# Optimization experiments

Hardware: AMD Instinct MI355X
Metric: run time of the kernel (lower is better)

## Reference

```python
import jax, jax.numpy as jnp
import numpy as np

B = 65536

def setup_inputs() -> dict:
    key = jax.random.key(0)
    ks = jax.random.split(key, 6)
    x = jax.random.normal(ks[0], (B, 784), dtype=jnp.float32)
    w_conv = jnp.ones((3, 3), dtype=jnp.float32)  # Parameter(ones((3,3)))
    w1 = jax.random.normal(ks[1], (676, 256), dtype=jnp.float32) * 0.04
    b1 = jax.random.normal(ks[2], (256,), dtype=jnp.float32) * 0.01
    w2 = jax.random.normal(ks[3], (256, 10), dtype=jnp.float32) * 0.06
    b2 = jax.random.normal(ks[4], (10,), dtype=jnp.float32) * 0.01
    return {"x": x, "w_conv": w_conv, "w1": w1, "b1": b1, "w2": w2, "b2": b2}

def reference(x, w_conv, w1, b1, w2, b2):
    b = x.shape[0]
    img = x.reshape(b, 1, 28, 28)
    # Convolve() is cross-correlation (no kernel flip), 'VALID': 28->26
    kern = w_conv.reshape(1, 1, 3, 3)
    conv = jax.lax.conv_general_dilated(
        img, kern, window_strides=(1, 1), padding='VALID',
        dimension_numbers=('NCHW', 'OIHW', 'NCHW'))  # (B,1,26,26)
    feat = conv.reshape(b, 676)
    h = jax.nn.relu(feat @ w1 + b1)  # (B,256)
    return h @ w2 + b2               # (B,10)
```

## Files before the change

### kernel.cpp

```cpp
#include <hip/hip_runtime.h>
#include <hip/hip_bf16.h>
#include <stdint.h>

typedef __bf16 bf16;
typedef __attribute__((ext_vector_type(8))) __bf16 bf16x8;
typedef __attribute__((ext_vector_type(4))) float f32x4;

#define KREAL 784
#define NTILES 25
#define TROW   40
#define TILE_ELEMS (256 * TROW)

#define GLOBAL_AS __attribute__((address_space(1)))
#define LDS_AS    __attribute__((address_space(3)))

__global__ __launch_bounds__(256) void prep_w1tt(const float* __restrict__ w_conv,
                                                 const float* __restrict__ w1,
                                                 bf16* __restrict__ W) {
    const int tile = blockIdx.x / TROW;
    const int kk   = blockIdx.x % TROW;
    const int n    = threadIdx.x;
    const int k    = tile * 32 + kk;
    float s = 0.0f;
    if (kk < 32 && k < KREAL) {
        const int r = k / 28, c = k % 28;
        #pragma unroll
        for (int di = 0; di < 3; ++di) {
            const int i = r - di;
            if (i < 0 || i >= 26) continue;
            #pragma unroll
            for (int dj = 0; dj < 3; ++dj) {
                const int j = c - dj;
                if (j < 0 || j >= 26) continue;
                s += w_conv[di * 3 + dj] * w1[(i * 26 + j) * 256 + n];
            }
        }
    }
    W[(size_t)tile * TILE_ELEMS + n * TROW + kk] = (bf16)s;
}

template <int CTRL>
__device__ __forceinline__ float dpp_add(float s) {
    int v = __builtin_amdgcn_update_dpp(0, __float_as_int(s), CTRL, 0xf, 0xf, false);
    return s + __int_as_float(v);
}

__global__ __launch_bounds__(256, 2) void fused_mlp(
    const float* __restrict__ x,
    const bf16*  __restrict__ W,
    const float* __restrict__ b1,
    const float* __restrict__ w2,
    const float* __restrict__ b2,
    float* __restrict__ out)
{
    __shared__ bf16  Bs[2][TILE_ELEMS];
    __shared__ float w2s[256][10];
    __shared__ float b1s[256];
    __shared__ float b2s[10];

    const int t    = threadIdx.x;
    const int wave = t >> 6;
    const int lane = t & 63;
    const int c    = lane & 15;
    const int q    = lane >> 4;

    const int row0 = blockIdx.x * 128;

    for (int i = t; i < 2560; i += 256) ((float*)w2s)[i] = w2[i];
    b1s[t] = b1[t];
    if (t < 10) b2s[t] = b2[t];

    const float* arow0 = x + (size_t)(row0 + wave * 32 + c) * KREAL + q * 8;
    const float* arow1 = arow0 + (size_t)16 * KREAL;
    const bf16* bsrc = W + (size_t)(wave * 5) * 512 + lane * 8;

    f32x4 acc[2][16];
    #pragma unroll
    for (int mt = 0; mt < 2; ++mt)
        #pragma unroll
        for (int nt = 0; nt < 16; ++nt)
            acc[mt][nt] = (f32x4){0.f, 0.f, 0.f, 0.f};

    #pragma unroll
    for (int j = 0; j < 5; ++j) {
        __builtin_amdgcn_global_load_lds(
            (const GLOBAL_AS void*)(bsrc + j * 512),
            (LDS_AS void*)((char*)&Bs[0][0] + (wave * 5 + j) * 1024), 16, 0, 0);
    }
    float4 f0a = *(const float4*)arow0, f0b = *(const float4*)(arow0 + 4);
    float4 f1a = *(const float4*)arow1, f1b = *(const float4*)(arow1 + 4);
    bf16x8 a0, a1;
    a0[0] = (bf16)f0a.x; a0[1] = (bf16)f0a.y; a0[2] = (bf16)f0a.z; a0[3] = (bf16)f0a.w;
    a0[4] = (bf16)f0b.x; a0[5] = (bf16)f0b.y; a0[6] = (bf16)f0b.z; a0[7] = (bf16)f0b.w;
    a1[0] = (bf16)f1a.x; a1[1] = (bf16)f1a.y; a1[2] = (bf16)f1a.z; a1[3] = (bf16)f1a.w;
    a1[4] = (bf16)f1b.x; a1[5] = (bf16)f1b.y; a1[6] = (bf16)f1b.z; a1[7] = (bf16)f1b.w;
    __syncthreads();

    #pragma unroll 1
    for (int it = 0; it < NTILES; ++it) {
        const int cur = it & 1;
        const bool more = (it + 1) < NTILES;

        if (more) {
            const bf16* bs = bsrc + (size_t)(it + 1) * TILE_ELEMS;
            char* bd = (char*)&Bs[cur ^ 1][0] + wave * 5 * 1024;
            #pragma unroll
            for (int j = 0; j < 5; ++j) {
                __builtin_amdgcn_global_load_lds(
                    (const GLOBAL_AS void*)(bs + j * 512),
                    (LDS_AS void*)(bd + j * 1024), 16, 0, 0);
            }
            const int kn = (it + 1) * 32;
            if (kn + q * 8 < KREAL) {
                const float* p0 = arow0 + kn;
                const float* p1 = arow1 + kn;
                f0a = *(const float4*)p0; f0b = *(const float4*)(p0 + 4);
                f1a = *(const float4*)p1; f1b = *(const float4*)(p1 + 4);
            } else {
                f0a = f0b = f1a = f1b = (float4){0.f, 0.f, 0.f, 0.f};
            }
        }

        #pragma unroll
        for (int nt = 0; nt < 16; ++nt) {
            bf16x8 b = *(const bf16x8*)&Bs[cur][(nt * 16 + c) * TROW + q * 8];
            acc[0][nt] = __builtin_amdgcn_mfma_f32_16x16x32_bf16(a0, b, acc[0][nt], 0, 0, 0);
            acc[1][nt] = __builtin_amdgcn_mfma_f32_16x16x32_bf16(a1, b, acc[1][nt], 0, 0, 0);
        }

        if (more) {
            a0[0] = (bf16)f0a.x; a0[1] = (bf16)f0a.y; a0[2] = (bf16)f0a.z; a0[3] = (bf16)f0a.w;
            a0[4] = (bf16)f0b.x; a0[5] = (bf16)f0b.y; a0[6] = (bf16)f0b.z; a0[7] = (bf16)f0b.w;
            a1[0] = (bf16)f1a.x; a1[1] = (bf16)f1a.y; a1[2] = (bf16)f1a.z; a1[3] = (bf16)f1a.w;
            a1[4] = (bf16)f1b.x; a1[5] = (bf16)f1b.y; a1[6] = (bf16)f1b.z; a1[7] = (bf16)f1b.w;
        }

        __syncthreads();
    }

    float bl[16];
    #pragma unroll
    for (int nt = 0; nt < 16; ++nt) bl[nt] = b1s[nt * 16 + c];

    #pragma unroll
    for (int mt = 0; mt < 2; ++mt)
        #pragma unroll
        for (int nt = 0; nt < 16; ++nt)
            #pragma unroll
            for (int r = 0; r < 4; ++r) {
                float v = acc[mt][nt][r] + bl[nt];
                acc[mt][nt][r] = v > 0.f ? v : 0.f;
            }

    #pragma unroll 1
    for (int j = 0; j < 10; ++j) {
        float wj[16];
        #pragma unroll
        for (int nt = 0; nt < 16; ++nt) wj[nt] = w2s[nt * 16 + c][j];
        const float b2j = b2s[j];
        #pragma unroll
        for (int mt = 0; mt < 2; ++mt)
            #pragma unroll
            for (int r = 0; r < 4; ++r) {
                float s = 0.f;
                #pragma unroll
                for (int nt = 0; nt < 16; ++nt) s += acc[mt][nt][r] * wj[nt];
                s = dpp_add<0xB1>(s);
                s = dpp_add<0x4E>(s);
                s = dpp_add<0x124>(s);
                s = dpp_add<0x128>(s);
                if (c == j) {
                    const int row = row0 + wave * 32 + mt * 16 + q * 4 + r;
                    out[(size_t)row * 10 + j] = s + b2j;
                }
            }
    }
}

extern "C" void kernel_launch(void* const* d_in, const int* in_sizes, int n_in,
                              void* d_out, int out_size, void* d_ws, size_t ws_size,
                              hipStream_t stream) {
    const float* x  = (const float*)d_in[0];
    const float* wc = (const float*)d_in[1];
    const float* w1 = (const float*)d_in[2];
    const float* b1 = (const float*)d_in[3];
    const float* w2 = (const float*)d_in[4];
    const float* b2 = (const float*)d_in[5];
    float* out = (float*)d_out;
    bf16* W = (bf16*)d_ws;

    prep_w1tt<<<dim3(NTILES * TROW), dim3(256), 0, stream>>>(wc, w1, W);
    fused_mlp<<<dim3(65536 / 128), dim3(256), 0, stream>>>(x, W, b1, w2, b2, out);
}
```

Measured before the change: 312.5 us.

## Prefetch activation rows two K-tiles ahead with explicit waitcnt barriers

Deepens the activation prefetch from one to two tiles ahead, using ping-pong float4 register sets and a loop unrolled by two. It also replaces __syncthreads with hand-placed s_waitcnt vmcnt plus s_barrier, so the newest global loads can stay in flight across the barrier. Out-of-range K chunks are now read at offset 0 and multiplied by a zero mask instead of branching. This uses more registers and relies on exact vmcnt accounting for correctness.

```diff
diff --git a/kernel.cpp b/kernel.cpp
--- a/kernel.cpp
+++ b/kernel.cpp
@@ -81,62 +81,89 @@
         for (int nt = 0; nt < 16; ++nt)
             acc[mt][nt] = (f32x4){0.f, 0.f, 0.f, 0.f};
 
+    float4 E0, E1, E2, E3, O0, O1, O2, O3;
+    bf16x8 a0, a1;
+
     #pragma unroll
     for (int j = 0; j < 5; ++j) {
         __builtin_amdgcn_global_load_lds(
             (const GLOBAL_AS void*)(bsrc + j * 512),
             (LDS_AS void*)((char*)&Bs[0][0] + (wave * 5 + j) * 1024), 16, 0, 0);
     }
-    float4 f0a = *(const float4*)arow0, f0b = *(const float4*)(arow0 + 4);
-    float4 f1a = *(const float4*)arow1, f1b = *(const float4*)(arow1 + 4);
-    bf16x8 a0, a1;
-    a0[0] = (bf16)f0a.x; a0[1] = (bf16)f0a.y; a0[2] = (bf16)f0a.z; a0[3] = (bf16)f0a.w;
-    a0[4] = (bf16)f0b.x; a0[5] = (bf16)f0b.y; a0[6] = (bf16)f0b.z; a0[7] = (bf16)f0b.w;
-    a1[0] = (bf16)f1a.x; a1[1] = (bf16)f1a.y; a1[2] = (bf16)f1a.z; a1[3] = (bf16)f1a.w;
-    a1[4] = (bf16)f1b.x; a1[5] = (bf16)f1b.y; a1[6] = (bf16)f1b.z; a1[7] = (bf16)f1b.w;
-    __syncthreads();
+    E0 = *(const float4*)arow0;        E1 = *(const float4*)(arow0 + 4);
+    E2 = *(const float4*)arow1;        E3 = *(const float4*)(arow1 + 4);
+    O0 = *(const float4*)(arow0 + 32); O1 = *(const float4*)(arow0 + 36);
+    O2 = *(const float4*)(arow1 + 32); O3 = *(const float4*)(arow1 + 36);
+    a0[0] = (bf16)E0.x; a0[1] = (bf16)E0.y; a0[2] = (bf16)E0.z; a0[3] = (bf16)E0.w;
+    a0[4] = (bf16)E1.x; a0[5] = (bf16)E1.y; a0[6] = (bf16)E1.z; a0[7] = (bf16)E1.w;
+    a1[0] = (bf16)E2.x; a1[1] = (bf16)E2.y; a1[2] = (bf16)E2.z; a1[3] = (bf16)E2.w;
+    a1[4] = (bf16)E3.x; a1[5] = (bf16)E3.y; a1[6] = (bf16)E3.z; a1[7] = (bf16)E3.w;
+    asm volatile("s_waitcnt vmcnt(4) lgkmcnt(0)" ::: "memory");
+    __builtin_amdgcn_sched_barrier(0);
+    __builtin_amdgcn_s_barrier();
+    __builtin_amdgcn_sched_barrier(0);
+
+#define KSTEP(IT, CUR, P0, P1, P2, P3, Q0, Q1, Q2, Q3)                         \
+    do {                                                                       \
+        const int  it_    = (IT);                                              \
+        const bool more_  = (it_ + 1) < NTILES;                                \
+        const bool more2_ = (it_ + 2) < NTILES;                                \
+        if (more_) {                 \
+            const bf16* bs_ = bsrc + (size_t)(it_ + 1) * TILE_ELEMS;           \
+            char* bd_ = (char*)&Bs[(CUR) ^ 1][0] + wave * 5 * 1024;            \
+            _Pragma("unroll")                                                  \
+            for (int j = 0; j < 5; ++j) {                                      \
+                __builtin_amdgcn_global_load_lds(                              \
+                    (const GLOBAL_AS void*)(bs_ + j * 512),                    \
+                    (LDS_AS void*)(bd_ + j * 1024), 16, 0, 0);                 \
+            }                                                                  \
+        }                                                                      \
+        if (more2_) {                         \
+            const int kn_   = (it_ + 2) * 32;                                  \
+            const int koff_ = (kn_ + q * 8 < KREAL) ? kn_ : 0;                 \
+            Q0 = *(const float4*)(arow0 + koff_);                              \
+            Q1 = *(const float4*)(arow0 + koff_ + 4);                          \
+            Q2 = *(const float4*)(arow1 + koff_);                              \
+            Q3 = *(const float4*)(arow1 + koff_ + 4);                          \
+        }                                                                      \
+        {                                            \
+            const bf16* bb_ = &Bs[(CUR)][0] + c * TROW + q * 8;                \
+            _Pragma("unroll")                                                  \
+            for (int nt = 0; nt < 16; ++nt) {                                  \
+                bf16x8 b_ = *(const bf16x8*)(bb_ + nt * 16 * TROW);            \
+                acc[0][nt] = __builtin_amdgcn_mfma_f32_16x16x32_bf16(          \
+                    a0, b_, acc[0][nt], 0, 0, 0);                              \
+                acc[1][nt] = __builtin_amdgcn_mfma_f32_16x16x32_bf16(          \
+                    a1, b_, acc[1][nt], 0, 0, 0);                              \
+            }                                                                  \
+        }                                                                      \
+        if (more_) {                \
+            const float okm_ = ((it_ + 1) * 32 + q * 8 < KREAL) ? 1.f : 0.f;   \
+            a0[0] = (bf16)(P0.x * okm_); a0[1] = (bf16)(P0.y * okm_);          \
+            a0[2] = (bf16)(P0.z * okm_); a0[3] = (bf16)(P0.w * okm_);          \
+            a0[4] = (bf16)(P1.x * okm_); a0[5] = (bf16)(P1.y * okm_);          \
+            a0[6] = (bf16)(P1.z * okm_); a0[7] = (bf16)(P1.w * okm_);          \
+            a1[0] = (bf16)(P2.x * okm_); a1[1] = (bf16)(P2.y * okm_);          \
+            a1[2] = (bf16)(P2.z * okm_); a1[3] = (bf16)(P2.w * okm_);          \
+            a1[4] = (bf16)(P3.x * okm_); a1[5] = (bf16)(P3.y * okm_);          \
+            a1[6] = (bf16)(P3.z * okm_); a1[7] = (bf16)(P3.w * okm_);          \
+        }                                                                      \
+        if (more_) {                    \
+            if (more2_) asm volatile("s_waitcnt vmcnt(4)" ::: "memory");       \
+            else        asm volatile("s_waitcnt vmcnt(0)" ::: "memory");       \
+            __builtin_amdgcn_sched_barrier(0);                                 \
+            __builtin_amdgcn_s_barrier();                                      \
+            __builtin_amdgcn_sched_barrier(0);                                 \
+        }                                                                      \
+    } while (0)
 
     #pragma unroll 1
-    for (int it = 0; it < NTILES; ++it) {
-        const int cur = it & 1;
-        const bool more = (it + 1) < NTILES;
-
-        if (more) {
-            const bf16* bs = bsrc + (size_t)(it + 1) * TILE_ELEMS;
-            char* bd = (char*)&Bs[cur ^ 1][0] + wave * 5 * 1024;
-            #pragma unroll
-            for (int j = 0; j < 5; ++j) {
-                __builtin_amdgcn_global_load_lds(
-                    (const GLOBAL_AS void*)(bs + j * 512),
-                    (LDS_AS void*)(bd + j * 1024), 16, 0, 0);
-            }
-            const int kn = (it + 1) * 32;
-            if (kn + q * 8 < KREAL) {
-                const float* p0 = arow0 + kn;
-                const float* p1 = arow1 + kn;
-                f0a = *(const float4*)p0; f0b = *(const float4*)(p0 + 4);
-                f1a = *(const float4*)p1; f1b = *(const float4*)(p1 + 4);
-            } else {
-                f0a = f0b = f1a = f1b = (float4){0.f, 0.f, 0.f, 0.f};
-            }
-        }
-
-        #pragma unroll
-        for (int nt = 0; nt < 16; ++nt) {
-            bf16x8 b = *(const bf16x8*)&Bs[cur][(nt * 16 + c) * TROW + q * 8];
-            acc[0][nt] = __builtin_amdgcn_mfma_f32_16x16x32_bf16(a0, b, acc[0][nt], 0, 0, 0);
-            acc[1][nt] = __builtin_amdgcn_mfma_f32_16x16x32_bf16(a1, b, acc[1][nt], 0, 0, 0);
-        }
-
-        if (more) {
-            a0[0] = (bf16)f0a.x; a0[1] = (bf16)f0a.y; a0[2] = (bf16)f0a.z; a0[3] = (bf16)f0a.w;
-            a0[4] = (bf16)f0b.x; a0[5] = (bf16)f0b.y; a0[6] = (bf16)f0b.z; a0[7] = (bf16)f0b.w;
-            a1[0] = (bf16)f1a.x; a1[1] = (bf16)f1a.y; a1[2] = (bf16)f1a.z; a1[3] = (bf16)f1a.w;
-            a1[4] = (bf16)f1b.x; a1[5] = (bf16)f1b.y; a1[6] = (bf16)f1b.z; a1[7] = (bf16)f1b.w;
-        }
-
-        __syncthreads();
-    }
+    for (int base = 0; base < NTILES - 1; base += 2) {
+        KSTEP(base,     0, O0, O1, O2, O3, E0, E1, E2, E3);
+        KSTEP(base + 1, 1, E0, E1, E2, E3, O0, O1, O2, O3);
+    }
+    KSTEP(NTILES - 1, 0, O0, O1, O2, O3, E0, E1, E2, E3);
+#undef KSTEP
 
     float bl[16];
     #pragma unroll
```

After: 315.8 us. About the same (+1.1%).

## Split waves into 64-row pairs sharing rows, halving N per wave

Applied to the files above, without the earlier changes.

Waves are regrouped into pairs that each cover 64 rows. Within a pair, each wave computes half of the 256 hidden columns over 4 M-tiles, so a wave now does 4x8 MFMAs per tile instead of 2x16. Each B fragment read from LDS is reused across four A tiles, which halves LDS B reads per MFMA. The cost is that each wave loads four A rows instead of two, so every x row is fetched by both waves of the pair and global A traffic doubles. The second layer's partial sums are combined across the pair through LDS, which adds a barrier.

```diff
diff --git a/kernel.cpp b/kernel.cpp
--- a/kernel.cpp
+++ b/kernel.cpp
@@ -43,6 +43,13 @@
 __device__ __forceinline__ float dpp_add(float s) {
     int v = __builtin_amdgcn_update_dpp(0, __float_as_int(s), CTRL, 0xf, 0xf, false);
     return s + __int_as_float(v);
+}
+
+__device__ __forceinline__ bf16x8 cvt8(float4 lo, float4 hi) {
+    bf16x8 r;
+    r[0] = (bf16)lo.x; r[1] = (bf16)lo.y; r[2] = (bf16)lo.z; r[3] = (bf16)lo.w;
+    r[4] = (bf16)hi.x; r[5] = (bf16)hi.y; r[6] = (bf16)hi.z; r[7] = (bf16)hi.w;
+    return r;
 }
 
 __global__ __launch_bounds__(256, 2) void fused_mlp(
@@ -63,6 +70,8 @@
     const int lane = t & 63;
     const int c    = lane & 15;
     const int q    = lane >> 4;
+    const int pair = wave >> 1;
+    const int nh   = wave & 1;
 
     const int row0 = blockIdx.x * 128;
 
@@ -70,15 +79,14 @@
     b1s[t] = b1[t];
     if (t < 10) b2s[t] = b2[t];
 
-    const float* arow0 = x + (size_t)(row0 + wave * 32 + c) * KREAL + q * 8;
-    const float* arow1 = arow0 + (size_t)16 * KREAL;
+    const float* ar = x + (size_t)(row0 + pair * 64 + c) * KREAL + q * 8;
     const bf16* bsrc = W + (size_t)(wave * 5) * 512 + lane * 8;
 
-    f32x4 acc[2][16];
-    #pragma unroll
-    for (int mt = 0; mt < 2; ++mt)
-        #pragma unroll
-        for (int nt = 0; nt < 16; ++nt)
+    f32x4 acc[4][8];
+    #pragma unroll
+    for (int mt = 0; mt < 4; ++mt)
+        #pragma unroll
+        for (int nt = 0; nt < 8; ++nt)
             acc[mt][nt] = (f32x4){0.f, 0.f, 0.f, 0.f};
 
     #pragma unroll
@@ -87,13 +95,16 @@
             (const GLOBAL_AS void*)(bsrc + j * 512),
             (LDS_AS void*)((char*)&Bs[0][0] + (wave * 5 + j) * 1024), 16, 0, 0);
     }
-    float4 f0a = *(const float4*)arow0, f0b = *(const float4*)(arow0 + 4);
-    float4 f1a = *(const float4*)arow1, f1b = *(const float4*)(arow1 + 4);
-    bf16x8 a0, a1;
-    a0[0] = (bf16)f0a.x; a0[1] = (bf16)f0a.y; a0[2] = (bf16)f0a.z; a0[3] = (bf16)f0a.w;
-    a0[4] = (bf16)f0b.x; a0[5] = (bf16)f0b.y; a0[6] = (bf16)f0b.z; a0[7] = (bf16)f0b.w;
-    a1[0] = (bf16)f1a.x; a1[1] = (bf16)f1a.y; a1[2] = (bf16)f1a.z; a1[3] = (bf16)f1a.w;
-    a1[4] = (bf16)f1b.x; a1[5] = (bf16)f1b.y; a1[6] = (bf16)f1b.z; a1[7] = (bf16)f1b.w;
+    float4 fa[4], fb[4];
+    #pragma unroll
+    for (int mt = 0; mt < 4; ++mt) {
+        const float* p = ar + (size_t)(mt * 16) * KREAL;
+        fa[mt] = *(const float4*)p;
+        fb[mt] = *(const float4*)(p + 4);
+    }
+    bf16x8 a[4];
+    #pragma unroll
+    for (int mt = 0; mt < 4; ++mt) a[mt] = cvt8(fa[mt], fb[mt]);
     __syncthreads();
 
     #pragma unroll 1
@@ -112,68 +123,98 @@
             }
             const int kn = (it + 1) * 32;
             if (kn + q * 8 < KREAL) {
-                const float* p0 = arow0 + kn;
-                const float* p1 = arow1 + kn;
-                f0a = *(const float4*)p0; f0b = *(const float4*)(p0 + 4);
-                f1a = *(const float4*)p1; f1b = *(const float4*)(p1 + 4);
+                #pragma unroll
+                for (int mt = 0; mt < 4; ++mt) {
+                    const float* p = ar + (size_t)(mt * 16) * KREAL + kn;
+                    fa[mt] = *(const float4*)p;
+                    fb[mt] = *(const float4*)(p + 4);
+                }
             } else {
-                f0a = f0b = f1a = f1b = (float4){0.f, 0.f, 0.f, 0.f};
-            }
-        }
-
-        #pragma unroll
-        for (int nt = 0; nt < 16; ++nt) {
-            bf16x8 b = *(const bf16x8*)&Bs[cur][(nt * 16 + c) * TROW + q * 8];
-            acc[0][nt] = __builtin_amdgcn_mfma_f32_16x16x32_bf16(a0, b, acc[0][nt], 0, 0, 0);
-            acc[1][nt] = __builtin_amdgcn_mfma_f32_16x16x32_bf16(a1, b, acc[1][nt], 0, 0, 0);
+                #pragma unroll
+                for (int mt = 0; mt < 4; ++mt)
+                    fa[mt] = fb[mt] = (float4){0.f, 0.f, 0.f, 0.f};
+            }
+        }
+
+        #pragma unroll
+        for (int nt = 0; nt < 8; ++nt) {
+            bf16x8 b = *(const bf16x8*)&Bs[cur][((nh * 8 + nt) * 16 + c) * TROW + q * 8];
+            #pragma unroll
+            for (int mt = 0; mt < 4; ++mt)
+                acc[mt][nt] = __builtin_amdgcn_mfma_f32_16x16x32_bf16(
+                    a[mt], b, acc[mt][nt], 0, 0, 0);
         }
 
         if (more) {
-            a0[0] = (bf16)f0a.x; a0[1] = (bf16)f0a.y; a0[2] = (bf16)f0a.z; a0[3] = (bf16)f0a.w;
-            a0[4] = (bf16)f0b.x; a0[5] = (bf16)f0b.y; a0[6] = (bf16)f0b.z; a0[7] = (bf16)f0b.w;
-            a1[0] = (bf16)f1a.x; a1[1] = (bf16)f1a.y; a1[2] = (bf16)f1a.z; a1[3] = (bf16)f1a.w;
-            a1[4] = (bf16)f1b.x; a1[5] = (bf16)f1b.y; a1[6] = (bf16)f1b.z; a1[7] = (bf16)f1b.w;
+            #pragma unroll
+            for (int mt = 0; mt < 4; ++mt) a[mt] = cvt8(fa[mt], fb[mt]);
         }
 
         __syncthreads();
     }
 
-    float bl[16];
-    #pragma unroll
-    for (int nt = 0; nt < 16; ++nt) bl[nt] = b1s[nt * 16 + c];
-
-    #pragma unroll
-    for (int mt = 0; mt < 2; ++mt)
-        #pragma unroll
-        for (int nt = 0; nt < 16; ++nt)
+    float bl[8];
+    #pragma unroll
+    for (int nt = 0; nt < 8; ++nt) bl[nt] = b1s[nh * 128 + nt * 16 + c];
+
+    #pragma unroll
+    for (int mt = 0; mt < 4; ++mt)
+        #pragma unroll
+        for (int nt = 0; nt < 8; ++nt)
             #pragma unroll
             for (int r = 0; r < 4; ++r) {
                 float v = acc[mt][nt][r] + bl[nt];
                 acc[mt][nt][r] = v > 0.f ? v : 0.f;
             }
 
+    float keep[4][4];
+    #pragma unroll
+    for (int mt = 0; mt < 4; ++mt)
+        #pragma unroll
+        for (int r = 0; r < 4; ++r) keep[mt][r] = 0.f;
+
     #pragma unroll 1
     for (int j = 0; j < 10; ++j) {
-        float wj[16];
-        #pragma unroll
-        for (int nt = 0; nt < 16; ++nt) wj[nt] = w2s[nt * 16 + c][j];
-        const float b2j = b2s[j];
-        #pragma unroll
-        for (int mt = 0; mt < 2; ++mt)
+        float wj[8];
+        #pragma unroll
+        for (int nt = 0; nt < 8; ++nt) wj[nt] = w2s[nh * 128 + nt * 16 + c][j];
+        #pragma unroll
+        for (int mt = 0; mt < 4; ++mt)
             #pragma unroll
             for (int r = 0; r < 4; ++r) {
                 float s = 0.f;
                 #pragma unroll
-                for (int nt = 0; nt < 16; ++nt) s += acc[mt][nt][r] * wj[nt];
+                for (int nt = 0; nt < 8; ++nt) s += acc[mt][nt][r] * wj[nt];
                 s = dpp_add<0xB1>(s);
                 s = dpp_add<0x4E>(s);
                 s = dpp_add<0x124>(s);
                 s = dpp_add<0x128>(s);
-                if (c == j) {
-                    const int row = row0 + wave * 32 + mt * 16 + q * 4 + r;
-                    out[(size_t)row * 10 + j] = s + b2j;
+                if (c == j) keep[mt][r] = s;
+            }
+    }
+
+    float* part = (float*)&Bs[0][0];
+    if (nh == 1) {
+        #pragma unroll
+        for (int mt = 0; mt < 4; ++mt)
+            #pragma unroll
+            for (int r = 0; r < 4; ++r)
+                if (c < 10)
+                    part[((((pair * 4 + mt) * 4 + r) * 4 + q) << 4) + c] = keep[mt][r];
+    }
+    __syncthreads();
+    if (nh == 0) {
+        #pragma unroll
+        for (int mt = 0; mt < 4; ++mt)
+            #pragma unroll
+            for (int r = 0; r < 4; ++r)
+                if (c < 10) {
+                    const int row = row0 + pair * 64 + mt * 16 + q * 4 + r;
+                    out[(size_t)row * 10 + c] =
+                        keep[mt][r] +
+                        part[((((pair * 4 + mt) * 4 + r) * 4 + q) << 4) + c] +
+                        b2s[c];
                 }
-            }
     }
 }
 
```

Result: no change. 315.8 us (+1.1%).
